# Optimization experiments

Measured on AMD Instinct MI355X. Metric: run time of the kernel, lower is better.

The kernel has to match this reference:

```python
import math
import jax, jax.numpy as jnp
import numpy as np

B, S, D = 2, 2048, 1024
N_HEADS, D_KV = 16, 64
INNER = N_HEADS * D_KV
NUM_BUCKETS = 32
MAX_DISTANCE = 128


def _relative_position_bucket(relative_position, num_buckets=NUM_BUCKETS, max_distance=MAX_DISTANCE):
    # bidirectional (encoder) variant
    nb = num_buckets // 2
    rel_buckets = (relative_position > 0).astype(jnp.int32) * nb
    rp = jnp.abs(relative_position)
    max_exact = nb // 2
    is_small = rp < max_exact
    rp_safe = jnp.maximum(rp, 1)  # avoid log(0); selected away by where
    rp_if_large = max_exact + (
        jnp.log(rp_safe.astype(jnp.float32) / max_exact)
        / math.log(max_distance / max_exact)
        * (nb - max_exact)
    ).astype(jnp.int32)
    rp_if_large = jnp.minimum(rp_if_large, nb - 1)
    return rel_buckets + jnp.where(is_small, rp, rp_if_large)


def compute_bias(rel_bias, q_len, k_len):
    ctx = jnp.arange(q_len)[:, None]
    mem = jnp.arange(k_len)[None, :]
    buckets = _relative_position_bucket(mem - ctx)  # [q_len, k_len]
    values = rel_bias[buckets]                      # [q_len, k_len, H]
    return jnp.transpose(values, (2, 0, 1))[None]   # [1, H, q_len, k_len]


def setup_inputs() -> dict:
    key = jax.random.key(0)
    ks = jax.random.split(key, 6)
    s = 1.0 / math.sqrt(D)
    return {
        "hidden_states": jax.random.normal(ks[0], (B, S, D), jnp.float32),
        "wq": jax.random.normal(ks[1], (D, INNER), jnp.float32) * s,
        "wk": jax.random.normal(ks[2], (D, INNER), jnp.float32) * s,
        "wv": jax.random.normal(ks[3], (D, INNER), jnp.float32) * s,
        "wo": jax.random.normal(ks[4], (INNER, D), jnp.float32) * s,
        "rel_bias": jax.random.normal(ks[5], (NUM_BUCKETS, N_HEADS), jnp.float32) * 0.1,
    }


def reference(hidden_states, wq, wk, wv, wo, rel_bias):
    b, s, _ = hidden_states.shape

    def shape(x):  # [b, s, inner] -> [b, h, s, d_kv]
        return x.reshape(b, s, N_HEADS, D_KV).transpose(0, 2, 1, 3)

    q = shape(hidden_states @ wq)  # note: T5 has NO 1/sqrt(d) scaling
    k = shape(hidden_states @ wk)
    v = shape(hidden_states @ wv)

    scores = jnp.einsum("bhqd,bhkd->bhqk", q, k)
    position_bias = compute_bias(rel_bias, s, s)
    scores = scores + position_bias
    attn = jax.nn.softmax(scores.astype(jnp.float32), axis=-1).astype(scores.dtype)

    out = jnp.einsum("bhqk,bhkd->bhqd", attn, v)
    out = out.transpose(0, 2, 1, 3).reshape(b, s, INNER)
    return out @ wo
```

## Files before the change

kernel.cpp:

```cpp
#include <hip/hip_runtime.h>
#include <hip/hip_bf16.h>

#define B_ 2
#define S_ 2048
#define D_ 1024
#define H_ 16
#define DKV_ 64
#define INNER_ 1024
#define M_ (B_*S_)

typedef unsigned short ushort_t;
typedef unsigned int u32;
typedef __bf16 bf16x8 __attribute__((ext_vector_type(8)));
typedef __bf16 bf16x4 __attribute__((ext_vector_type(4)));
typedef float f32x4 __attribute__((ext_vector_type(4)));

#define VMCNT0 asm volatile("s_waitcnt vmcnt(0)" ::: "memory")
#define VMCNT4 asm volatile("s_waitcnt vmcnt(4)" ::: "memory")
#define LOG2E 1.4426950408889634f

__device__ __forceinline__ unsigned short f2bf(float f) {
    unsigned int u = __builtin_bit_cast(unsigned int, f);
    unsigned int r = (u + 0x7fffu + ((u >> 16) & 1u)) >> 16;
    return (unsigned short)r;
}

__device__ __forceinline__ void gload16(const ushort_t* g, ushort_t* l) {
    __builtin_amdgcn_global_load_lds(
        (const __attribute__((address_space(1))) u32*)g,
        (__attribute__((address_space(3))) u32*)l, 16, 0, 0);
}

__global__ __launch_bounds__(256) void cvt_bf16(const float* __restrict__ in,
                                                unsigned short* __restrict__ out, int n) {
    int i = (blockIdx.x * 256 + threadIdx.x) * 4;
    if (i < n) {
        float4 v = *(const float4*)&in[i];
        ushort4 o;
        o.x = f2bf(v.x); o.y = f2bf(v.y); o.z = f2bf(v.z); o.w = f2bf(v.w);
        *(ushort4*)&out[i] = o;
    }
}

__global__ __launch_bounds__(256) void transp_bf16(
        const float* __restrict__ s0, const float* __restrict__ s1,
        const float* __restrict__ s2, const float* __restrict__ s3,
        unsigned short* __restrict__ d0, unsigned short* __restrict__ d1,
        unsigned short* __restrict__ d2, unsigned short* __restrict__ d3) {
    const float* srcs[4] = {s0, s1, s2, s3};
    unsigned short* dsts[4] = {d0, d1, d2, d3};
    const float* src = srcs[blockIdx.z];
    unsigned short* dst = dsts[blockIdx.z];
    __shared__ float t[64][65];
    int k0 = blockIdx.y * 64, n0 = blockIdx.x * 64;
    for (int i = threadIdx.x; i < 4096; i += 256) {
        int r = i >> 6, c = i & 63;
        t[r][c] = src[(k0 + r) * 1024 + n0 + c];
    }
    __syncthreads();
    for (int i = threadIdx.x; i < 4096; i += 256) {
        int r = i >> 6, c = i & 63;
        dst[(n0 + r) * 1024 + k0 + c] = f2bf(t[c][r]);
    }
}

__global__ __launch_bounds__(256) void bias_kernel(const float* __restrict__ rb,
                                                   float* __restrict__ btab) {
    int idx = blockIdx.x * 256 + threadIdx.x;
    int h = idx >> 12, pos = idx & 4095;
    int rel = pos - 2048;
    int bb = rel > 0 ? 16 : 0;
    int rp = rel < 0 ? -rel : rel;
    int bucket;
    if (rp < 8) bucket = bb + rp;
    else {
        int v = 8 + (int)(logf((float)rp * 0.125f) / 2.7725887f * 8.0f);
        bucket = bb + (v < 15 ? v : 15);
    }
    btab[idx] = rb[bucket * 16 + h] * LOG2E;
}

__global__ __launch_bounds__(256) void gemm_qkv(const ushort_t* __restrict__ A,
        const ushort_t* __restrict__ WQ, const ushort_t* __restrict__ WK, const ushort_t* __restrict__ WV,
        ushort_t* __restrict__ Qb, ushort_t* __restrict__ Kb, ushort_t* __restrict__ Vtb) {
    __shared__ alignas(16) ushort_t As[128][64];
    __shared__ alignas(16) ushort_t Bs[128][64];
    int tid = threadIdx.x, wid = tid >> 6, lane = tid & 63;
    int linear = blockIdx.x;
    int swz = (linear & 7) * 96 + (linear >> 3);
    int m0 = (swz / 24) * 128;
    int nblk = swz % 24;
    int sel = nblk >> 3;
    const ushort_t* Bt = sel == 0 ? WQ : (sel == 1 ? WK : WV);
    int n0 = (nblk & 7) * 128;
    int lr = lane & 15, lg = lane >> 4;
    int wm = (wid >> 1) * 64, wn = (wid & 1) * 64;
    int srow = tid >> 3, sp = tid & 7;
    int scol = (sp ^ (srow & 7)) * 8;
    int cR0 = (lg ^ (lr & 7)) * 8;
    int cR1 = ((4 + lg) ^ (lr & 7)) * 8;
    const ushort_t* Abase = A + (size_t)m0 * 1024 + scol;
    const ushort_t* Bbase = Bt + (size_t)n0 * 1024 + scol;
    f32x4 acc[4][4] = {};
    for (int kt = 0; kt < 1024; kt += 64) {
        #pragma unroll
        for (int j = 0; j < 4; ++j) {
            int row = j * 32 + srow;
            gload16(Abase + row * 1024 + kt, &As[0][0] + (j * 256 + tid) * 8);
            gload16(Bbase + row * 1024 + kt, &Bs[0][0] + (j * 256 + tid) * 8);
        }
        VMCNT0;
        __syncthreads();
        bf16x8 af[4][2], bfr[4][2];
        #pragma unroll
        for (int t = 0; t < 4; ++t) {
            af[t][0]  = *(const bf16x8*)&As[wm + t * 16 + lr][cR0];
            af[t][1]  = *(const bf16x8*)&As[wm + t * 16 + lr][cR1];
            bfr[t][0] = *(const bf16x8*)&Bs[wn + t * 16 + lr][cR0];
            bfr[t][1] = *(const bf16x8*)&Bs[wn + t * 16 + lr][cR1];
        }
        #pragma unroll
        for (int hh = 0; hh < 2; ++hh)
            #pragma unroll
            for (int i2 = 0; i2 < 4; ++i2)
                #pragma unroll
                for (int j2 = 0; j2 < 4; ++j2)
                    acc[i2][j2] = __builtin_amdgcn_mfma_f32_16x16x32_bf16(af[i2][hh], bfr[j2][hh], acc[i2][j2], 0, 0, 0);
        __syncthreads();
    }
    #pragma unroll
    for (int i2 = 0; i2 < 4; ++i2)
        #pragma unroll
        for (int j2 = 0; j2 < 4; ++j2) {
            int col = n0 + wn + j2 * 16 + lr;
            int hh = col >> 6, d = col & 63;
            if (sel < 2) {
                ushort_t* dst = sel == 0 ? Qb : Kb;
                #pragma unroll
                for (int r = 0; r < 4; ++r) {
                    int row = m0 + wm + i2 * 16 + lg * 4 + r;
                    int b = row >> 11, s = row & 2047;
                    dst[(((size_t)(b * H_ + hh) * S_ + s)) * DKV_ + d] = f2bf(acc[i2][j2][r]);
                }
            } else {
                int row0 = m0 + wm + i2 * 16 + lg * 4;
                int b = row0 >> 11, s0 = row0 & 2047;
                ushort4 sv;
                sv.x = f2bf(acc[i2][j2][0]); sv.y = f2bf(acc[i2][j2][1]);
                sv.z = f2bf(acc[i2][j2][2]); sv.w = f2bf(acc[i2][j2][3]);
                *(ushort4*)&Vtb[((size_t)(b * H_ + hh) * DKV_ + d) * S_ + s0] = sv;
            }
        }
}

__global__ __launch_bounds__(256) void gemm_out(const ushort_t* __restrict__ A,
                                                const ushort_t* __restrict__ Bt,
                                                float* __restrict__ C) {
    __shared__ alignas(16) ushort_t As[64][64];
    __shared__ alignas(16) ushort_t Bs[128][64];
    int tid = threadIdx.x, wid = tid >> 6, lane = tid & 63;
    int linear = blockIdx.x;
    int swz = (linear & 7) * 64 + (linear >> 3);
    int m0 = (swz >> 3) * 64, n0 = (swz & 7) * 128;
    int lr = lane & 15, lg = lane >> 4;
    int wn = wid * 32;
    int srow = tid >> 3, sp = tid & 7;
    int scol = (sp ^ (srow & 7)) * 8;
    int cR0 = (lg ^ (lr & 7)) * 8;
    int cR1 = ((4 + lg) ^ (lr & 7)) * 8;
    const ushort_t* Abase = A + (size_t)m0 * 1024 + scol;
    const ushort_t* Bbase = Bt + (size_t)n0 * 1024 + scol;
    f32x4 acc[4][2] = {};
    for (int kt = 0; kt < 1024; kt += 64) {
        #pragma unroll
        for (int j = 0; j < 2; ++j) {
            int row = j * 32 + srow;
            gload16(Abase + row * 1024 + kt, &As[0][0] + (j * 256 + tid) * 8);
        }
        #pragma unroll
        for (int j = 0; j < 4; ++j) {
            int row = j * 32 + srow;
            gload16(Bbase + row * 1024 + kt, &Bs[0][0] + (j * 256 + tid) * 8);
        }
        VMCNT0;
        __syncthreads();
        bf16x8 af[4][2], bfr[2][2];
        #pragma unroll
        for (int t = 0; t < 4; ++t) {
            af[t][0] = *(const bf16x8*)&As[t * 16 + lr][cR0];
            af[t][1] = *(const bf16x8*)&As[t * 16 + lr][cR1];
        }
        #pragma unroll
        for (int j = 0; j < 2; ++j) {
            bfr[j][0] = *(const bf16x8*)&Bs[wn + j * 16 + lr][cR0];
            bfr[j][1] = *(const bf16x8*)&Bs[wn + j * 16 + lr][cR1];
        }
        #pragma unroll
        for (int hh = 0; hh < 2; ++hh)
            #pragma unroll
            for (int i2 = 0; i2 < 4; ++i2)
                #pragma unroll
                for (int j2 = 0; j2 < 2; ++j2)
                    acc[i2][j2] = __builtin_amdgcn_mfma_f32_16x16x32_bf16(af[i2][hh], bfr[j2][hh], acc[i2][j2], 0, 0, 0);
        __syncthreads();
    }
    #pragma unroll
    for (int i2 = 0; i2 < 4; ++i2)
        #pragma unroll
        for (int j2 = 0; j2 < 2; ++j2)
            #pragma unroll
            for (int r = 0; r < 4; ++r)
                C[(size_t)(m0 + i2 * 16 + lg * 4 + r) * 1024 + n0 + wn + j2 * 16 + lr] = acc[i2][j2][r];
}

__global__ __launch_bounds__(256) void flash_attn(const ushort_t* __restrict__ Q,
                                                  const ushort_t* __restrict__ Kg,
                                                  const ushort_t* __restrict__ Vt,
                                                  const float* __restrict__ bias_tab,
                                                  ushort_t* __restrict__ Out) {
    __shared__ alignas(16) ushort_t Ks[3][64][64];
    __shared__ alignas(16) ushort_t Vs[3][64][64];
    __shared__ alignas(16) ushort_t Ps[4][16][64];
    __shared__ float LbS[2176];
    int tid = threadIdx.x, wid = tid >> 6, lane = tid & 63;
    int linear = blockIdx.x;
    int swz = (linear & 7) * 64 + (linear >> 3);
    int bh = swz >> 4, qblk = swz & 15;
    int h = bh & 15, b = bh >> 4;
    int q0b = qblk * 128;
    int q0w = q0b + wid * 32;
    int lr = lane & 15, lg = lane >> 4;

    {
        const float* bsrc = bias_tab + h * 4096 + 2048 - q0b - 127;
        for (int i = tid; i < 2175; i += 256) LbS[i] = bsrc[i];
    }

    const ushort_t* Qbase = Q + ((size_t)bh * S_ + q0w) * DKV_;
    bf16x8 qA0 = *(const bf16x8*)&Qbase[lr * DKV_ + lg * 8];
    bf16x8 qA1 = *(const bf16x8*)&Qbase[lr * DKV_ + 32 + lg * 8];
    bf16x8 qB0 = *(const bf16x8*)&Qbase[(16 + lr) * DKV_ + lg * 8];
    bf16x8 qB1 = *(const bf16x8*)&Qbase[(16 + lr) * DKV_ + 32 + lg * 8];

    int srow = tid >> 3, sp = tid & 7;
    int kc = (sp ^ (srow & 7)) * 8;
    const ushort_t* Ksrc = Kg + (size_t)bh * S_ * DKV_ + kc;
    const ushort_t* Vsrc = Vt + (size_t)bh * DKV_ * S_ + kc;
    int c0 = (lg ^ (lr & 7)) * 8;
    int c1 = ((4 + lg) ^ (lr & 7)) * 8;
    int pxor = (lr & 7) << 4;

    f32x4 oA[4] = {}, oB[4] = {};
    f32x4 lpA = {}, lpB = {};
    float mA = -INFINITY, mB = -INFINITY;
    const int bbA = 127 - wid * 32 + 4 * lg - lr;
    const int bbB = bbA - 16;

    auto stage = [&](int bi, int kt) {
        ushort_t* kb = &Ks[bi][0][0];
        ushort_t* vb = &Vs[bi][0][0];
        gload16(Ksrc + (size_t)(kt + srow) * 64,      kb + tid * 8);
        gload16(Ksrc + (size_t)(kt + 32 + srow) * 64, kb + 2048 + tid * 8);
        gload16(Vsrc + (size_t)srow * S_ + kt,        vb + tid * 8);
        gload16(Vsrc + (size_t)(32 + srow) * S_ + kt, vb + 2048 + tid * 8);
    };

    stage(0, 0);
    stage(1, 64);
    VMCNT4;
    __syncthreads();
    int cur = 0;
    for (int t = 0; t < 32; ++t) {
        const int kt = t * 64;
        if (t < 30) {
            int nxt = cur + 2; if (nxt >= 3) nxt -= 3;
            stage(nxt, kt + 128);
        }
        f32x4 sA[4] = {}, sB[4] = {};
        #pragma unroll
        for (int nt = 0; nt < 4; ++nt) {
            bf16x8 kf0 = *(const bf16x8*)&Ks[cur][nt * 16 + lr][c0];
            bf16x8 kf1 = *(const bf16x8*)&Ks[cur][nt * 16 + lr][c1];
            sA[nt] = __builtin_amdgcn_mfma_f32_16x16x32_bf16(kf0, qA0, sA[nt], 0, 0, 0);
            sA[nt] = __builtin_amdgcn_mfma_f32_16x16x32_bf16(kf1, qA1, sA[nt], 0, 0, 0);
            sB[nt] = __builtin_amdgcn_mfma_f32_16x16x32_bf16(kf0, qB0, sB[nt], 0, 0, 0);
            sB[nt] = __builtin_amdgcn_mfma_f32_16x16x32_bf16(kf1, qB1, sB[nt], 0, 0, 0);
        }
        char* pbase = (char*)&Ps[wid][lr][0];
        bf16x8 pfA0, pfA1;
        {
            float p[4][4]; float mnt[4];
            const int bi = kt + bbA;
            #pragma unroll
            for (int nt = 0; nt < 4; ++nt) {
                #pragma unroll
                for (int r = 0; r < 4; ++r)
                    p[nt][r] = fmaf(sA[nt][r], LOG2E, LbS[bi + nt * 16 + r]);
                mnt[nt] = fmaxf(fmaxf(p[nt][0], p[nt][1]), fmaxf(p[nt][2], p[nt][3]));
            }
            float mt = fmaxf(fmaxf(mnt[0], mnt[1]), fmaxf(mnt[2], mnt[3]));
            mt = fmaxf(mt, __shfl_xor(mt, 16));
            mt = fmaxf(mt, __shfl_xor(mt, 32));
            if (!__all(mt <= mA + 8.f)) {
                float mnew = fmaxf(mA, mt);
                float sc = __builtin_amdgcn_exp2f(mA - mnew);
                mA = mnew;
                lpA *= sc;
                #pragma unroll
                for (int dt = 0; dt < 4; ++dt) oA[dt] *= sc;
            }
            #pragma unroll
            for (int nt = 0; nt < 4; ++nt) {
                #pragma unroll
                for (int r = 0; r < 4; ++r) {
                    p[nt][r] = __builtin_amdgcn_exp2f(p[nt][r] - mA);
                    lpA[r] += p[nt][r];
                }
                bf16x4 pv;
                pv[0] = (__bf16)p[nt][0]; pv[1] = (__bf16)p[nt][1];
                pv[2] = (__bf16)p[nt][2]; pv[3] = (__bf16)p[nt][3];
                *(bf16x4*)(pbase + ((nt * 32 + lg * 8) ^ pxor)) = pv;
            }
            pfA0 = *(const bf16x8*)(pbase + ((lg * 16) ^ pxor));
            pfA1 = *(const bf16x8*)(pbase + ((64 + lg * 16) ^ pxor));
        }
        bf16x8 pfB0, pfB1;
        {
            float p[4][4]; float mnt[4];
            const int bi = kt + bbB;
            #pragma unroll
            for (int nt = 0; nt < 4; ++nt) {
                #pragma unroll
                for (int r = 0; r < 4; ++r)
                    p[nt][r] = fmaf(sB[nt][r], LOG2E, LbS[bi + nt * 16 + r]);
                mnt[nt] = fmaxf(fmaxf(p[nt][0], p[nt][1]), fmaxf(p[nt][2], p[nt][3]));
            }
            float mt = fmaxf(fmaxf(mnt[0], mnt[1]), fmaxf(mnt[2], mnt[3]));
            mt = fmaxf(mt, __shfl_xor(mt, 16));
            mt = fmaxf(mt, __shfl_xor(mt, 32));
            if (!__all(mt <= mB + 8.f)) {
                float mnew = fmaxf(mB, mt);
                float sc = __builtin_amdgcn_exp2f(mB - mnew);
                mB = mnew;
                lpB *= sc;
                #pragma unroll
                for (int dt = 0; dt < 4; ++dt) oB[dt] *= sc;
            }
            #pragma unroll
            for (int nt = 0; nt < 4; ++nt) {
                #pragma unroll
                for (int r = 0; r < 4; ++r) {
                    p[nt][r] = __builtin_amdgcn_exp2f(p[nt][r] - mB);
                    lpB[r] += p[nt][r];
                }
                bf16x4 pv;
                pv[0] = (__bf16)p[nt][0]; pv[1] = (__bf16)p[nt][1];
                pv[2] = (__bf16)p[nt][2]; pv[3] = (__bf16)p[nt][3];
                *(bf16x4*)(pbase + ((nt * 32 + lg * 8) ^ pxor)) = pv;
            }
            pfB0 = *(const bf16x8*)(pbase + ((lg * 16) ^ pxor));
            pfB1 = *(const bf16x8*)(pbase + ((64 + lg * 16) ^ pxor));
        }
        #pragma unroll
        for (int dt = 0; dt < 4; ++dt) {
            bf16x8 vf0 = *(const bf16x8*)&Vs[cur][dt * 16 + lr][c0];
            bf16x8 vf1 = *(const bf16x8*)&Vs[cur][dt * 16 + lr][c1];
            oA[dt] = __builtin_amdgcn_mfma_f32_16x16x32_bf16(vf0, pfA0, oA[dt], 0, 0, 0);
            oA[dt] = __builtin_amdgcn_mfma_f32_16x16x32_bf16(vf1, pfA1, oA[dt], 0, 0, 0);
            oB[dt] = __builtin_amdgcn_mfma_f32_16x16x32_bf16(vf0, pfB0, oB[dt], 0, 0, 0);
            oB[dt] = __builtin_amdgcn_mfma_f32_16x16x32_bf16(vf1, pfB1, oB[dt], 0, 0, 0);
        }
        if (t < 30) { VMCNT4; } else { VMCNT0; }
        __syncthreads();
        ++cur; if (cur >= 3) cur = 0;
    }
    float lA = (lpA[0] + lpA[1]) + (lpA[2] + lpA[3]);
    lA += __shfl_xor(lA, 16); lA += __shfl_xor(lA, 32);
    float lB = (lpB[0] + lpB[1]) + (lpB[2] + lpB[3]);
    lB += __shfl_xor(lB, 16); lB += __shfl_xor(lB, 32);
    {
        float linv = 1.f / lA;
        char* pbase = (char*)&Ps[wid][lr][0];
        #pragma unroll
        for (int dt = 0; dt < 4; ++dt) {
            bf16x4 ov;
            ov[0] = (__bf16)(oA[dt][0] * linv); ov[1] = (__bf16)(oA[dt][1] * linv);
            ov[2] = (__bf16)(oA[dt][2] * linv); ov[3] = (__bf16)(oA[dt][3] * linv);
            *(bf16x4*)(pbase + ((dt * 32 + lg * 8) ^ pxor)) = ov;
        }
        int row = lane >> 2, seg = lane & 3;
        int rxor = (row & 7) << 4;
        char* rbase = (char*)&Ps[wid][row][0];
        uint4 v0 = *(uint4*)(rbase + ((seg * 32) ^ rxor));
        uint4 v1 = *(uint4*)(rbase + ((seg * 32 + 16) ^ rxor));
        ushort_t* dst = Out + (size_t)(b * S_ + q0w + row) * INNER_ + h * DKV_ + seg * 16;
        *(uint4*)&dst[0] = v0;
        *(uint4*)&dst[8] = v1;
    }
    {
        float linv = 1.f / lB;
        char* pbase = (char*)&Ps[wid][lr][0];
        #pragma unroll
        for (int dt = 0; dt < 4; ++dt) {
            bf16x4 ov;
            ov[0] = (__bf16)(oB[dt][0] * linv); ov[1] = (__bf16)(oB[dt][1] * linv);
            ov[2] = (__bf16)(oB[dt][2] * linv); ov[3] = (__bf16)(oB[dt][3] * linv);
            *(bf16x4*)(pbase + ((dt * 32 + lg * 8) ^ pxor)) = ov;
        }
        int row = lane >> 2, seg = lane & 3;
        int rxor = (row & 7) << 4;
        char* rbase = (char*)&Ps[wid][row][0];
        uint4 v0 = *(uint4*)(rbase + ((seg * 32) ^ rxor));
        uint4 v1 = *(uint4*)(rbase + ((seg * 32 + 16) ^ rxor));
        ushort_t* dst = Out + (size_t)(b * S_ + q0w + 16 + row) * INNER_ + h * DKV_ + seg * 16;
        *(uint4*)&dst[0] = v0;
        *(uint4*)&dst[8] = v1;
    }
}

extern "C" void kernel_launch(void* const* d_in, const int* in_sizes, int n_in,
                              void* d_out, int out_size, void* d_ws, size_t ws_size,
                              hipStream_t stream) {
    const float* hs = (const float*)d_in[0];
    const float* wq = (const float*)d_in[1];
    const float* wk = (const float*)d_in[2];
    const float* wv = (const float*)d_in[3];
    const float* wo = (const float*)d_in[4];
    const float* rb = (const float*)d_in[5];

    char* ws = (char*)d_ws;
    unsigned short* Abf = (unsigned short*)(ws);
    unsigned short* Wqt = (unsigned short*)(ws + (8u  << 20));
    unsigned short* Wkt = (unsigned short*)(ws + (10u << 20));
    unsigned short* Wvt = (unsigned short*)(ws + (12u << 20));
    unsigned short* Wot = (unsigned short*)(ws + (14u << 20));
    unsigned short* Qb  = (unsigned short*)(ws + (16u << 20));
    unsigned short* Kb  = (unsigned short*)(ws + (24u << 20));
    unsigned short* Vtb = (unsigned short*)(ws + (32u << 20));
    unsigned short* AOb = (unsigned short*)(ws + (40u << 20));
    float*          Btab = (float*)(ws + (48u << 20));

    cvt_bf16<<<4096, 256, 0, stream>>>(hs, Abf, M_ * D_);
    transp_bf16<<<dim3(16, 16, 4), 256, 0, stream>>>(wq, wk, wv, wo, Wqt, Wkt, Wvt, Wot);
    bias_kernel<<<256, 256, 0, stream>>>(rb, Btab);

    gemm_qkv<<<768, 256, 0, stream>>>(Abf, Wqt, Wkt, Wvt, Qb, Kb, Vtb);

    flash_attn<<<512, 256, 0, stream>>>(Qb, Kb, Vtb, Btab, AOb);

    gemm_out<<<512, 256, 0, stream>>>(AOb, Wot, (float*)d_out);
}
```

Measured before the change: 137.8 us.

## Load V fragments directly to registers with double buffering and MFMA priority hints

V tiles now go straight from global memory into per-thread register fragments, double-buffered across iterations, instead of being staged through LDS, which removes the V shared buffers and their LDS reads. The loop is unrolled by two so the register buffers alternate, and the waitcnt thresholds are adjusted to match. The PV MFMAs for the A half are moved up to interleave with the B-half softmax, and s_setprio raises wave priority around MFMA blocks. Launch bounds request three blocks per CU. The trade-off is higher register pressure and uncoalesced direct global loads of V.

Measured after the change: 238.3 us. +72.9%, slower.

```diff
diff --git a/kernel.cpp b/kernel.cpp
--- a/kernel.cpp
+++ b/kernel.cpp
@@ -16,7 +16,6 @@
 typedef float f32x4 __attribute__((ext_vector_type(4)));
 
 #define VMCNT0 asm volatile("s_waitcnt vmcnt(0)" ::: "memory")
-#define VMCNT4 asm volatile("s_waitcnt vmcnt(4)" ::: "memory")
 #define LOG2E 1.4426950408889634f
 
 __device__ __forceinline__ unsigned short f2bf(float f) {
@@ -213,13 +212,14 @@
                 C[(size_t)(m0 + i2 * 16 + lg * 4 + r) * 1024 + n0 + wn + j2 * 16 + lr] = acc[i2][j2][r];
 }
 
-__global__ __launch_bounds__(256) void flash_attn(const ushort_t* __restrict__ Q,
-                                                  const ushort_t* __restrict__ Kg,
-                                                  const ushort_t* __restrict__ Vt,
-                                                  const float* __restrict__ bias_tab,
-                                                  ushort_t* __restrict__ Out) {
+struct VTile { bf16x8 f[4][2]; };
+
+__global__ __launch_bounds__(256, 3) void flash_attn(const ushort_t* __restrict__ Q,
+                                                     const ushort_t* __restrict__ Kg,
+                                                     const ushort_t* __restrict__ Vt,
+                                                     const float* __restrict__ bias_tab,
+                                                     ushort_t* __restrict__ Out) {
     __shared__ alignas(16) ushort_t Ks[3][64][64];
-    __shared__ alignas(16) ushort_t Vs[3][64][64];
     __shared__ alignas(16) ushort_t Ps[4][16][64];
     __shared__ float LbS[2176];
     int tid = threadIdx.x, wid = tid >> 6, lane = tid & 63;
@@ -245,7 +245,7 @@
     int srow = tid >> 3, sp = tid & 7;
     int kc = (sp ^ (srow & 7)) * 8;
     const ushort_t* Ksrc = Kg + (size_t)bh * S_ * DKV_ + kc;
-    const ushort_t* Vsrc = Vt + (size_t)bh * DKV_ * S_ + kc;
+    const ushort_t* Vfrag = Vt + ((size_t)bh * DKV_ + lr) * S_ + lg * 8;
     int c0 = (lg ^ (lr & 7)) * 8;
     int c1 = ((4 + lg) ^ (lr & 7)) * 8;
     int pxor = (lr & 7) << 4;
@@ -256,27 +256,37 @@
     const int bbA = 127 - wid * 32 + 4 * lg - lr;
     const int bbB = bbA - 16;
 
-    auto stage = [&](int bi, int kt) {
+    auto stageK = [&](int bi, int kt) {
         ushort_t* kb = &Ks[bi][0][0];
-        ushort_t* vb = &Vs[bi][0][0];
         gload16(Ksrc + (size_t)(kt + srow) * 64,      kb + tid * 8);
         gload16(Ksrc + (size_t)(kt + 32 + srow) * 64, kb + 2048 + tid * 8);
-        gload16(Vsrc + (size_t)srow * S_ + kt,        vb + tid * 8);
-        gload16(Vsrc + (size_t)(32 + srow) * S_ + kt, vb + 2048 + tid * 8);
     };
-
-    stage(0, 0);
-    stage(1, 64);
-    VMCNT4;
+    auto loadV = [&](int kt, VTile& v) {
+        #pragma unroll
+        for (int dt = 0; dt < 4; ++dt) {
+            const ushort_t* vp = Vfrag + (size_t)dt * 16 * S_ + kt;
+            v.f[dt][0] = *(const bf16x8*)vp;
+            v.f[dt][1] = *(const bf16x8*)(vp + 32);
+        }
+    };
+
+    VTile vA, vB;
+    loadV(0, vA);
+    stageK(0, 0);
+    stageK(1, 64);
+    asm volatile("s_waitcnt vmcnt(2)" ::: "memory");
     __syncthreads();
-    int cur = 0;
-    for (int t = 0; t < 32; ++t) {
+
+    auto body = [&](int t, int cur, VTile& vuse, VTile& vnext) {
         const int kt = t * 64;
+        if (t < 31) loadV(kt + 64, vnext);
         if (t < 30) {
-            int nxt = cur + 2; if (nxt >= 3) nxt -= 3;
-            stage(nxt, kt + 128);
-        }
+            int nb = cur + 2; if (nb >= 3) nb -= 3;
+            stageK(nb, kt + 128);
+        }
+        __builtin_amdgcn_sched_barrier(0);
         f32x4 sA[4] = {}, sB[4] = {};
+        __builtin_amdgcn_s_setprio(1);
         #pragma unroll
         for (int nt = 0; nt < 4; ++nt) {
             bf16x8 kf0 = *(const bf16x8*)&Ks[cur][nt * 16 + lr][c0];
@@ -286,6 +296,7 @@
             sB[nt] = __builtin_amdgcn_mfma_f32_16x16x32_bf16(kf0, qB0, sB[nt], 0, 0, 0);
             sB[nt] = __builtin_amdgcn_mfma_f32_16x16x32_bf16(kf1, qB1, sB[nt], 0, 0, 0);
         }
+        __builtin_amdgcn_s_setprio(0);
         char* pbase = (char*)&Ps[wid][lr][0];
         bf16x8 pfA0, pfA1;
         {
@@ -324,6 +335,13 @@
             pfA0 = *(const bf16x8*)(pbase + ((lg * 16) ^ pxor));
             pfA1 = *(const bf16x8*)(pbase + ((64 + lg * 16) ^ pxor));
         }
+        __builtin_amdgcn_s_setprio(1);
+        #pragma unroll
+        for (int dt = 0; dt < 4; ++dt) {
+            oA[dt] = __builtin_amdgcn_mfma_f32_16x16x32_bf16(vuse.f[dt][0], pfA0, oA[dt], 0, 0, 0);
+            oA[dt] = __builtin_amdgcn_mfma_f32_16x16x32_bf16(vuse.f[dt][1], pfA1, oA[dt], 0, 0, 0);
+        }
+        __builtin_amdgcn_s_setprio(0);
         bf16x8 pfB0, pfB1;
         {
             float p[4][4]; float mnt[4];
@@ -361,19 +379,29 @@
             pfB0 = *(const bf16x8*)(pbase + ((lg * 16) ^ pxor));
             pfB1 = *(const bf16x8*)(pbase + ((64 + lg * 16) ^ pxor));
         }
+        __builtin_amdgcn_s_setprio(1);
         #pragma unroll
         for (int dt = 0; dt < 4; ++dt) {
-            bf16x8 vf0 = *(const bf16x8*)&Vs[cur][dt * 16 + lr][c0];
-            bf16x8 vf1 = *(const bf16x8*)&Vs[cur][dt * 16 + lr][c1];
-            oA[dt] = __builtin_amdgcn_mfma_f32_16x16x32_bf16(vf0, pfA0, oA[dt], 0, 0, 0);
-            oA[dt] = __builtin_amdgcn_mfma_f32_16x16x32_bf16(vf1, pfA1, oA[dt], 0, 0, 0);
-            oB[dt] = __builtin_amdgcn_mfma_f32_16x16x32_bf16(vf0, pfB0, oB[dt], 0, 0, 0);
-            oB[dt] = __builtin_amdgcn_mfma_f32_16x16x32_bf16(vf1, pfB1, oB[dt], 0, 0, 0);
-        }
-        if (t < 30) { VMCNT4; } else { VMCNT0; }
-        __syncthreads();
-        ++cur; if (cur >= 3) cur = 0;
-    }
+            oB[dt] = __builtin_amdgcn_mfma_f32_16x16x32_bf16(vuse.f[dt][0], pfB0, oB[dt], 0, 0, 0);
+            oB[dt] = __builtin_amdgcn_mfma_f32_16x16x32_bf16(vuse.f[dt][1], pfB1, oB[dt], 0, 0, 0);
+        }
+        __builtin_amdgcn_s_setprio(0);
+        if (t < 30) {
+            asm volatile("s_waitcnt vmcnt(10)" ::: "memory");
+            __syncthreads();
+        } else if (t == 30) {
+            asm volatile("s_waitcnt vmcnt(8)" ::: "memory");
+            __syncthreads();
+        }
+    };
+
+    for (int tt = 0; tt < 32; tt += 2) {
+        int c0i = tt % 3;
+        int c1i = c0i + 1; if (c1i >= 3) c1i = 0;
+        body(tt,     c0i, vA, vB);
+        body(tt + 1, c1i, vB, vA);
+    }
+
     float lA = (lpA[0] + lpA[1]) + (lpA[2] + lpA[3]);
     lA += __shfl_xor(lA, 16); lA += __shfl_xor(lA, 32);
     float lB = (lpB[0] + lpB[1]) + (lpB[2] + lpB[3]);
```
